# Kernel tuning notes

Hardware: AMD Instinct MI355X
Metric: run time of the kernel (lower is better)

## Reference

```python
import jax, jax.numpy as jnp
import numpy as np

B, L, D = 4, 1024, 1024
H, DK, DV = 16, 64, 64
HID = 4 * D
EPS = 1e-5


def layer_norm(x, w, b):
    m = x.mean(-1, keepdims=True)
    v = ((x - m) ** 2).mean(-1, keepdims=True)
    return (x - m) * jax.lax.rsqrt(v + EPS) * w + b


def sln(hl, w, ln_w, ln_b, gamma, beta):
    # Self-modulated LayerNorm: gamma * w * LN(hl) + beta * w
    return gamma * w * layer_norm(hl, ln_w, ln_b) + beta * w


def setup_inputs() -> dict:
    key = jax.random.key(0)
    ks = jax.random.split(key, 20)
    s = 0.02
    inp = {
        "q": jax.random.normal(ks[0], (B, L, D), jnp.float32),
        "k": jax.random.normal(ks[1], (B, L, D), jnp.float32),
        "v": jax.random.normal(ks[2], (B, L, D), jnp.float32),
        "z": jax.random.normal(ks[3], (B, L, D), jnp.float32),
        # projections stored [in, out] (torch Linear applies x @ W.T + b)
        "wq_w": jax.random.normal(ks[4], (D, H * DK), jnp.float32) * s,
        "wq_b": jnp.zeros((H * DK,), jnp.float32),
        "wk_w": jax.random.normal(ks[5], (D, H * DK), jnp.float32) * s,
        "wk_b": jnp.zeros((H * DK,), jnp.float32),
        "wv_w": jax.random.normal(ks[6], (D, H * DV), jnp.float32) * s,
        "wv_b": jnp.zeros((H * DV,), jnp.float32),
        "fc_w": jax.random.normal(ks[7], (H * DV, D), jnp.float32) * s,
        "fc_b": jnp.zeros((D,), jnp.float32),
        "mlp1_w": jax.random.normal(ks[8], (D, HID), jnp.float32) * s,
        "mlp1_b": jnp.zeros((HID,), jnp.float32),
        "mlp2_w": jax.random.normal(ks[9], (HID, D), jnp.float32) * s,
        "mlp2_b": jnp.zeros((D,), jnp.float32),
        "ln1_w": jnp.ones((D,), jnp.float32),
        "ln1_b": jnp.zeros((D,), jnp.float32),
        "g1": jax.random.normal(ks[10], (1, 1, 1), jnp.float32),
        "b1": jax.random.normal(ks[11], (1, 1, 1), jnp.float32),
        "ln2_w": jnp.ones((D,), jnp.float32),
        "ln2_b": jnp.zeros((D,), jnp.float32),
        "g2": jax.random.normal(ks[12], (1, 1, 1), jnp.float32),
        "b2": jax.random.normal(ks[13], (1, 1, 1), jnp.float32),
    }
    return inp


def reference(q, k, v, z,
              wq_w, wq_b, wk_w, wk_b, wv_w, wv_b, fc_w, fc_b,
              mlp1_w, mlp1_b, mlp2_w, mlp2_b,
              ln1_w, ln1_b, g1, b1, ln2_w, ln2_b, g2, b2):
    scale = 1.0 / np.sqrt(DK).astype(np.float32)
    q = sln(q, z, ln1_w, ln1_b, g1, b1)
    residual = q
    qh = (q @ wq_w + wq_b).reshape(B, L, H, DK)
    kh = (k @ wk_w + wk_b).reshape(B, L, H, DK)
    vh = (v @ wv_w + wv_b).reshape(B, L, H, DV)
    # scores per (head, batch) matching torch layout (n_head*sz_b, Lq, Lk)
    attn = jnp.einsum("bqhd,bkhd->hbqk", qh, kh) * scale
    attn = jax.nn.softmax(attn, axis=-1)
    out = jnp.einsum("hbqk,bkhd->bqhd", attn, vh).reshape(B, L, H * DV)
    out = out @ fc_w + fc_b
    out = out + residual
    h = sln(out, z, ln2_w, ln2_b, g2, b2)
    h = jax.nn.gelu(h @ mlp1_w + mlp1_b, approximate=False)
    out = (h @ mlp2_w + mlp2_b) + out
    return out, attn.reshape(H * B, L, L)
```

## Files before the change

kernel.cpp:

```cpp
#include <hip/hip_runtime.h>
#include <math.h>

namespace {

constexpr int kL  = 1024;
constexpr int kD  = 1024;
constexpr int kB  = 4;
constexpr int kH  = 16;
constexpr int kDK = 64;
constexpr int kHID = 4096;

typedef unsigned short ushort_t;
typedef short  s16x8 __attribute__((ext_vector_type(8)));
typedef float  f32x4 __attribute__((ext_vector_type(4)));
typedef unsigned short u16x4 __attribute__((ext_vector_type(4)));

__device__ __forceinline__ ushort_t f2bf(float f) {
    unsigned u = __float_as_uint(f);
    unsigned r = u + 0x7fffu + ((u >> 16) & 1u);
    return (ushort_t)(r >> 16);
}

__device__ __forceinline__ void gld16(const void* g, void* l) {
    __builtin_amdgcn_global_load_lds((__attribute__((address_space(1))) void*)(g),
                                     (__attribute__((address_space(3))) void*)(l),
                                     16, 0, 0);
}

__device__ __forceinline__ float wred_sum(float v) {
    #pragma unroll
    for (int o = 32; o > 0; o >>= 1) v += __shfl_xor(v, o, 64);
    return v;
}

__global__ __launch_bounds__(256) void prep(
    const float* __restrict__ wq_w, const float* __restrict__ wk_w,
    const float* __restrict__ wv_w, const float* __restrict__ fc_w,
    ushort_t* __restrict__ wT4,
    const float* __restrict__ mlp1_w, ushort_t* __restrict__ m1T,
    const float* __restrict__ mlp2_w, ushort_t* __restrict__ m2T,
    const float* __restrict__ kx, const float* __restrict__ vx, ushort_t* __restrict__ kv,
    const float* __restrict__ q, const float* __restrict__ z,
    const float* __restrict__ ln1w, const float* __restrict__ ln1b,
    const float* __restrict__ g1, const float* __restrict__ b1,
    float* __restrict__ qp, ushort_t* __restrict__ qb)
{
    __shared__ float t[32][33];
    __shared__ float r1[4], r2[4];
    const int b = blockIdx.x;
    const int tid = threadIdx.x;
    if (b < 12288) {
        const float* src; ushort_t* dst; int R, C, bx, by;
        if (b < 4096) {
            int zz = b >> 10, idx = b & 1023;
            src = zz == 0 ? wq_w : zz == 1 ? wk_w : zz == 2 ? wv_w : fc_w;
            dst = wT4 + (size_t)zz * 1048576;
            R = 1024; C = 1024; bx = idx & 31; by = idx >> 5;
        } else if (b < 8192) {
            int idx = b - 4096;
            src = mlp1_w; dst = m1T; R = 1024; C = 4096;
            bx = idx & 127; by = idx >> 7;
        } else {
            int idx = b - 8192;
            src = mlp2_w; dst = m2T; R = 4096; C = 1024;
            bx = idx & 31; by = idx >> 5;
        }
        int c0 = bx * 32, rr0 = by * 32;
        int tx = tid & 31, ty = tid >> 5;
        #pragma unroll
        for (int i = 0; i < 4; i++) {
            int r = ty + i * 8;
            t[r][tx] = src[(size_t)(rr0 + r) * C + c0 + tx];
        }
        __syncthreads();
        #pragma unroll
        for (int i = 0; i < 4; i++) {
            int c = ty + i * 8;
            dst[(size_t)(c0 + c) * R + rr0 + tx] = f2bf(t[tx][c]);
        }
        return;
    }
    if (b < 20480) {
        int bb = b - 12288;
        bool isv = bb >= 4096;
        const float* src = isv ? vx : kx;
        ushort_t* dst = kv + (isv ? (size_t)4194304 : 0);
        int i = (bb & 4095) * 256 + tid;
        f32x4 v = ((const f32x4*)src)[i];
        u16x4 o; o[0] = f2bf(v[0]); o[1] = f2bf(v[1]); o[2] = f2bf(v[2]); o[3] = f2bf(v[3]);
        ((u16x4*)dst)[i] = o;
        return;
    }
    {
        const int row = b - 20480;
        const size_t base = (size_t)row * kD;
        float4 xv = ((const float4*)(q + base))[tid];
        float s  = xv.x + xv.y + xv.z + xv.w;
        float sq = xv.x * xv.x + xv.y * xv.y + xv.z * xv.z + xv.w * xv.w;
        float ws = wred_sum(s), wq = wred_sum(sq);
        int lane = tid & 63, wid = tid >> 6;
        if (lane == 0) { r1[wid] = ws; r2[wid] = wq; }
        __syncthreads();
        float st = r1[0] + r1[1] + r1[2] + r1[3];
        float qt = r2[0] + r2[1] + r2[2] + r2[3];
        float mean = st * (1.0f / kD);
        float var  = qt * (1.0f / kD) - mean * mean;
        float rs = rsqrtf(var + 1e-5f);
        float gv = g1[0], bv = b1[0];
        float4 zv = ((const float4*)(z + base))[tid];
        float4 wv = ((const float4*)ln1w)[tid];
        float4 lb = ((const float4*)ln1b)[tid];
        float4 o;
        o.x = zv.x * (gv * ((xv.x - mean) * rs * wv.x + lb.x) + bv);
        o.y = zv.y * (gv * ((xv.y - mean) * rs * wv.y + lb.y) + bv);
        o.z = zv.z * (gv * ((xv.z - mean) * rs * wv.z + lb.z) + bv);
        o.w = zv.w * (gv * ((xv.w - mean) * rs * wv.w + lb.w) + bv);
        ((float4*)(qp + base))[tid] = o;
        u16x4 ob; ob[0] = f2bf(o.x); ob[1] = f2bf(o.y); ob[2] = f2bf(o.z); ob[3] = f2bf(o.w);
        ((u16x4*)(qb + base))[tid] = ob;
    }
}

__global__ __launch_bounds__(256) void sln_kernel(
    const float* __restrict__ x, const float* __restrict__ x2, float* __restrict__ xw,
    const float* __restrict__ z,
    const float* __restrict__ lnw, const float* __restrict__ lnb,
    const float* __restrict__ g, const float* __restrict__ bt,
    float* __restrict__ outf, ushort_t* __restrict__ outb)
{
    const int row = blockIdx.x;
    const int tid = threadIdx.x;
    const size_t base = (size_t)row * kD;
    float4 xv = ((const float4*)(x + base))[tid];
    if (x2) {
        float4 a = ((const float4*)(x2 + base))[tid];
        xv.x += a.x; xv.y += a.y; xv.z += a.z; xv.w += a.w;
    }
    if (xw) ((float4*)(xw + base))[tid] = xv;
    float s  = xv.x + xv.y + xv.z + xv.w;
    float sq = xv.x * xv.x + xv.y * xv.y + xv.z * xv.z + xv.w * xv.w;
    __shared__ float r1[4], r2[4];
    float ws = wred_sum(s), wq = wred_sum(sq);
    int lane = tid & 63, wid = tid >> 6;
    if (lane == 0) { r1[wid] = ws; r2[wid] = wq; }
    __syncthreads();
    float st = r1[0] + r1[1] + r1[2] + r1[3];
    float qt = r2[0] + r2[1] + r2[2] + r2[3];
    float mean = st * (1.0f / kD);
    float var  = qt * (1.0f / kD) - mean * mean;
    float rs = rsqrtf(var + 1e-5f);
    float gv = g[0], bv = bt[0];
    float4 zv = ((const float4*)(z + base))[tid];
    float4 wv = ((const float4*)lnw)[tid];
    float4 lb = ((const float4*)lnb)[tid];
    float4 o;
    o.x = zv.x * (gv * ((xv.x - mean) * rs * wv.x + lb.x) + bv);
    o.y = zv.y * (gv * ((xv.y - mean) * rs * wv.y + lb.y) + bv);
    o.z = zv.z * (gv * ((xv.z - mean) * rs * wv.z + lb.z) + bv);
    o.w = zv.w * (gv * ((xv.w - mean) * rs * wv.w + lb.w) + bv);
    if (outf) ((float4*)(outf + base))[tid] = o;
    u16x4 ob; ob[0] = f2bf(o.x); ob[1] = f2bf(o.y); ob[2] = f2bf(o.z); ob[3] = f2bf(o.w);
    ((u16x4*)(outb + base))[tid] = ob;
}

__global__ __launch_bounds__(256) void addf4(
    float* __restrict__ dst, const float* __restrict__ src)
{
    int i = blockIdx.x * 256 + threadIdx.x;
    f32x4 d = ((const f32x4*)dst)[i];
    f32x4 s = ((const f32x4*)src)[i];
    d[0] += s[0]; d[1] += s[1]; d[2] += s[2]; d[3] += s[3];
    ((f32x4*)dst)[i] = d;
}

__global__ __launch_bounds__(256) void mgemm(
    const ushort_t* __restrict__ A, int lda,
    const ushort_t* __restrict__ Bt, int ldb,
    void* __restrict__ Cv, int ldc, int K,
    const float* __restrict__ bias, const float* __restrict__ res,
    float scale, int flags, int mode,
    const float* __restrict__ bias1, void* __restrict__ Cv2)
{
    __shared__ __align__(16) ushort_t As[128 * 32];
    __shared__ __align__(16) ushort_t Bs[128 * 32];
    if (mode == 2) {
        int zz = blockIdx.z;
        A  += (size_t)zz * (4096u * 1024u);
        Bt += (size_t)zz * (1024u * 1024u);
        Cv = (void*)((ushort_t*)Cv + (size_t)zz * (4096u * 1024u));
        if (zz == 1) bias = bias1;
    } else if (mode == 3) {
        int zz = blockIdx.z;
        A  += (size_t)zz * K;
        Bt += (size_t)zz * K;
        if (zz == 1) { Cv = Cv2; bias = nullptr; res = nullptr; flags = 0; }
    }
    float*    Cf = (float*)Cv;
    ushort_t* Cb = (ushort_t*)Cv;
    const int nx = gridDim.x, nwg = nx * gridDim.y;
    int f = blockIdx.y * nx + blockIdx.x;
    int rr = (f & 7) * (nwg >> 3) + (f >> 3);
    const int bx = rr % nx, by = rr / nx;
    const int tid = threadIdx.x;
    const int lane = tid & 63, w = tid >> 6;
    const int m0 = by * 128, n0 = bx * 128;
    const int r0 = tid >> 2;
    const int c0 = (tid & 3) ^ (r0 & 3);
    const ushort_t* Ag0 = A  + (size_t)(m0 + r0) * lda + c0 * 8;
    const ushort_t* Ag1 = Ag0 + (size_t)64 * lda;
    const ushort_t* Bg0 = Bt + (size_t)(n0 + r0) * ldb + c0 * 8;
    const ushort_t* Bg1 = Bg0 + (size_t)64 * ldb;
    char* AsW = (char*)As + w * 1024;
    char* BsW = (char*)Bs + w * 1024;
    const int wm = (w & 1) * 64, wn = (w >> 1) * 64;
    const int fn = lane & 15, q = lane >> 4;
    int aoff[4], boff[4];
    #pragma unroll
    for (int i = 0; i < 4; i++) {
        int ra = wm + i * 16 + fn;
        aoff[i] = (ra * 4 + (q ^ (ra & 3))) * 16;
        int rb = wn + i * 16 + fn;
        boff[i] = (rb * 4 + (q ^ (rb & 3))) * 16;
    }
    f32x4 acc[4][4] = {};
    for (int k0 = 0; k0 < K; k0 += 32) {
        gld16(Ag0 + k0, AsW);
        gld16(Ag1 + k0, AsW + 4096);
        gld16(Bg0 + k0, BsW);
        gld16(Bg1 + k0, BsW + 4096);
        __syncthreads();
        s16x8 af[4], bfr[4];
        #pragma unroll
        for (int i = 0; i < 4; i++) {
            af[i]  = *(const s16x8*)((const char*)As + aoff[i]);
            bfr[i] = *(const s16x8*)((const char*)Bs + boff[i]);
        }
        #pragma unroll
        for (int mi = 0; mi < 4; mi++)
            #pragma unroll
            for (int ni = 0; ni < 4; ni++)
                acc[mi][ni] = __builtin_amdgcn_mfma_f32_16x16x32_bf16(
                    af[mi], bfr[ni], acc[mi][ni], 0, 0, 0);
        __syncthreads();
    }
    #pragma unroll
    for (int mi = 0; mi < 4; mi++) {
        #pragma unroll
        for (int ni = 0; ni < 4; ni++) {
            #pragma unroll
            for (int r = 0; r < 4; r++) {
                int gm = m0 + wm + mi * 16 + q * 4 + r;
                int gn = n0 + wn + ni * 16 + fn;
                float v = acc[mi][ni][r] * scale;
                if (bias) v += (flags & 4) ? bias[gm] : bias[gn];
                if (flags & 1) v = 0.5f * v * (1.0f + erff(v * 0.70710678118654752f));
                if (res) v += res[(size_t)gm * ldc + gn];
                if (flags & 2) Cb[(size_t)gm * ldc + gn] = f2bf(v);
                else           Cf[(size_t)gm * ldc + gn] = v;
            }
        }
    }
}

__global__ __launch_bounds__(512) void fused_attn(
    const ushort_t* __restrict__ qh, const ushort_t* __restrict__ kh,
    const ushort_t* __restrict__ vT, float* __restrict__ attn,
    ushort_t* __restrict__ ctx)
{
    __shared__ __align__(16) char PlBuf[8 * 4096];
    __shared__ float redm[8][32];
    __shared__ float reds[8][32];
    const int orig = blockIdx.y * 32 + blockIdx.x;
    const int nf = (orig & 7) * 256 + (orig >> 3);
    const int p = nf >> 5, b = p & 3, h = p >> 2;
    const int m0 = (nf & 31) * 32;
    const int tid = threadIdx.x;
    const int lane = tid & 63, w = tid >> 6;
    const int fn = lane & 15, q = lane >> 4;
    const ushort_t* Qb = qh + (size_t)b * (kL * kD) + h * 64;
    const ushort_t* Kb = kh + (size_t)b * (kL * kD) + h * 64;
    float* Pp = attn + (size_t)p * kL * kL;

    f32x4 acc[2][8] = {};
    #pragma unroll
    for (int kk = 0; kk < 2; kk++) {
        s16x8 aq[2], bq[8];
        #pragma unroll
        for (int mi = 0; mi < 2; mi++)
            aq[mi] = *(const s16x8*)(Qb + (size_t)(m0 + mi * 16 + fn) * kD + kk * 32 + q * 8);
        #pragma unroll
        for (int ni = 0; ni < 8; ni++)
            bq[ni] = *(const s16x8*)(Kb + (size_t)(w * 128 + ni * 16 + fn) * kD + kk * 32 + q * 8);
        #pragma unroll
        for (int mi = 0; mi < 2; mi++)
            #pragma unroll
            for (int ni = 0; ni < 8; ni++)
                acc[mi][ni] = __builtin_amdgcn_mfma_f32_16x16x32_bf16(
                    aq[mi], bq[ni], acc[mi][ni], 0, 0, 0);
    }

    float mloc[2][4];
    #pragma unroll
    for (int mi = 0; mi < 2; mi++) {
        #pragma unroll
        for (int r = 0; r < 4; r++) {
            float m = -3.0e38f;
            #pragma unroll
            for (int ni = 0; ni < 8; ni++) {
                acc[mi][ni][r] *= 0.125f;
                m = fmaxf(m, acc[mi][ni][r]);
            }
            mloc[mi][r] = m;
        }
    }
    #pragma unroll
    for (int o = 1; o < 16; o <<= 1) {
        #pragma unroll
        for (int mi = 0; mi < 2; mi++)
            #pragma unroll
            for (int r = 0; r < 4; r++)
                mloc[mi][r] = fmaxf(mloc[mi][r], __shfl_xor(mloc[mi][r], o, 64));
    }
    if (fn == 0) {
        #pragma unroll
        for (int mi = 0; mi < 2; mi++)
            #pragma unroll
            for (int r = 0; r < 4; r++)
                redm[w][mi * 16 + q * 4 + r] = mloc[mi][r];
    }
    __syncthreads();
    #pragma unroll
    for (int mi = 0; mi < 2; mi++) {
        #pragma unroll
        for (int r = 0; r < 4; r++) {
            int row = mi * 16 + q * 4 + r;
            float m = redm[0][row];
            #pragma unroll
            for (int w2 = 1; w2 < 8; w2++) m = fmaxf(m, redm[w2][row]);
            float s = 0.f;
            #pragma unroll
            for (int ni = 0; ni < 8; ni++) {
                float e = __expf(acc[mi][ni][r] - m);
                acc[mi][ni][r] = e;
                s += e;
            }
            mloc[mi][r] = s;
        }
    }
    #pragma unroll
    for (int o = 1; o < 16; o <<= 1) {
        #pragma unroll
        for (int mi = 0; mi < 2; mi++)
            #pragma unroll
            for (int r = 0; r < 4; r++)
                mloc[mi][r] += __shfl_xor(mloc[mi][r], o, 64);
    }
    if (fn == 0) {
        #pragma unroll
        for (int mi = 0; mi < 2; mi++)
            #pragma unroll
            for (int r = 0; r < 4; r++)
                reds[w][mi * 16 + q * 4 + r] = mloc[mi][r];
    }
    __syncthreads();
    float inv[2][4];
    #pragma unroll
    for (int mi = 0; mi < 2; mi++) {
        #pragma unroll
        for (int r = 0; r < 4; r++) {
            int row = mi * 16 + q * 4 + r;
            float s = reds[0][row];
            #pragma unroll
            for (int w2 = 1; w2 < 8; w2++) s += reds[w2][row];
            inv[mi][r] = 1.0f / s;
        }
    }
    #pragma unroll
    for (int mi = 0; mi < 2; mi++)
        #pragma unroll
        for (int ni = 0; ni < 8; ni++)
            #pragma unroll
            for (int r = 0; r < 4; r++)
                __builtin_nontemporal_store(
                    acc[mi][ni][r] * inv[mi][r],
                    &Pp[(size_t)(m0 + mi * 16 + q * 4 + r) * kL + w * 128 + ni * 16 + fn]);

    const ushort_t* Vb = vT + (size_t)h * 64 * 4096 + (size_t)b * 1024;
    char* Plw = PlBuf + w * 4096;
    f32x4 acc2[2][4] = {};
    #pragma unroll
    for (int half = 0; half < 2; half++) {
        #pragma unroll
        for (int mi = 0; mi < 2; mi++)
            #pragma unroll
            for (int ni = 0; ni < 4; ni++)
                #pragma unroll
                for (int r = 0; r < 4; r++) {
                    int row = mi * 16 + q * 4 + r;
                    int cl  = ni * 16 + fn;
                    *(ushort_t*)(Plw + ((row * 128 + cl * 2) ^ ((row & 7) << 4)))
                        = f2bf(acc[mi][half * 4 + ni][r]);
                }
        #pragma unroll
        for (int kh2 = 0; kh2 < 2; kh2++) {
            int kk = half * 2 + kh2;
            s16x8 pa[2];
            #pragma unroll
            for (int mi = 0; mi < 2; mi++) {
                int row = mi * 16 + fn;
                pa[mi] = *(const s16x8*)(Plw +
                    ((row * 128 + (kh2 * 32 + q * 8) * 2) ^ ((row & 7) << 4)));
            }
            #pragma unroll
            for (int nj = 0; nj < 4; nj++) {
                s16x8 bv = *(const s16x8*)(Vb + (size_t)(nj * 16 + fn) * 4096 +
                                           w * 128 + kk * 32 + q * 8);
                #pragma unroll
                for (int mi = 0; mi < 2; mi++)
                    acc2[mi][nj] = __builtin_amdgcn_mfma_f32_16x16x32_bf16(
                        pa[mi], bv, acc2[mi][nj], 0, 0, 0);
            }
        }
    }
    #pragma unroll
    for (int mi = 0; mi < 2; mi++)
        #pragma unroll
        for (int nj = 0; nj < 4; nj++)
            #pragma unroll
            for (int r = 0; r < 4; r++)
                acc2[mi][nj][r] *= inv[mi][r];

    __syncthreads();
    float (*cred)[2048] = (float (*)[2048])PlBuf;
    if (w < 4) {
        #pragma unroll
        for (int mi = 0; mi < 2; mi++)
            #pragma unroll
            for (int nj = 0; nj < 4; nj++)
                #pragma unroll
                for (int r = 0; r < 4; r++)
                    cred[w][(mi * 16 + q * 4 + r) * 64 + nj * 16 + fn] = acc2[mi][nj][r];
    }
    __syncthreads();
    if (w >= 4) {
        #pragma unroll
        for (int mi = 0; mi < 2; mi++)
            #pragma unroll
            for (int nj = 0; nj < 4; nj++)
                #pragma unroll
                for (int r = 0; r < 4; r++)
                    cred[w - 4][(mi * 16 + q * 4 + r) * 64 + nj * 16 + fn] += acc2[mi][nj][r];
    }
    __syncthreads();
    {
        int idx0 = tid * 4;
        int row = idx0 >> 6, d0 = idx0 & 63;
        f32x4 s0 = *(const f32x4*)&cred[0][idx0];
        #pragma unroll
        for (int wb = 1; wb < 4; wb++) {
            f32x4 t = *(const f32x4*)&cred[wb][idx0];
            s0[0] += t[0]; s0[1] += t[1]; s0[2] += t[2]; s0[3] += t[3];
        }
        u16x4 o;
        o[0] = f2bf(s0[0]); o[1] = f2bf(s0[1]); o[2] = f2bf(s0[2]); o[3] = f2bf(s0[3]);
        *(u16x4*)(ctx + (size_t)b * (kL * kD) + (size_t)(m0 + row) * kD + h * 64 + d0) = o;
    }
}

}

extern "C" void kernel_launch(void* const* d_in, const int* in_sizes, int n_in,
                              void* d_out, int out_size, void* d_ws, size_t ws_size,
                              hipStream_t stream)
{
    (void)in_sizes; (void)n_in; (void)out_size; (void)ws_size;
    const float* q      = (const float*)d_in[0];
    const float* k      = (const float*)d_in[1];
    const float* v      = (const float*)d_in[2];
    const float* z      = (const float*)d_in[3];
    const float* wq_b   = (const float*)d_in[5];
    const float* wq_w   = (const float*)d_in[4];
    const float* wk_w   = (const float*)d_in[6];
    const float* wk_b   = (const float*)d_in[7];
    const float* wv_w   = (const float*)d_in[8];
    const float* wv_b   = (const float*)d_in[9];
    const float* fc_w   = (const float*)d_in[10];
    const float* fc_b   = (const float*)d_in[11];
    const float* mlp1_w = (const float*)d_in[12];
    const float* mlp1_b = (const float*)d_in[13];
    const float* mlp2_w = (const float*)d_in[14];
    const float* mlp2_b = (const float*)d_in[15];
    const float* ln1_w  = (const float*)d_in[16];
    const float* ln1_b  = (const float*)d_in[17];
    const float* g1     = (const float*)d_in[18];
    const float* b1     = (const float*)d_in[19];
    const float* ln2_w  = (const float*)d_in[20];
    const float* ln2_b  = (const float*)d_in[21];
    const float* g2     = (const float*)d_in[22];
    const float* b2     = (const float*)d_in[23];

    float* out0 = (float*)d_out;
    float* attn = (float*)d_out + (size_t)kB * kL * kD;

    char* arena = (char*)d_ws;
    const size_t MB = 1u << 20;
    float*    qp   = (float*)(arena);
    ushort_t* qb   = (ushort_t*)(arena + 16 * MB);
    ushort_t* kb   = (ushort_t*)(arena + 24 * MB);
    ushort_t* vb   = (ushort_t*)(arena + 32 * MB);
    ushort_t* qh   = (ushort_t*)(arena + 40 * MB);
    ushort_t* kh   = (ushort_t*)(arena + 48 * MB);
    ushort_t* vT   = (ushort_t*)(arena + 56 * MB);
    ushort_t* ctx  = (ushort_t*)(arena + 32 * MB);
    float*    fcP  = (float*)(arena + 16 * MB);
    ushort_t* h2   = (ushort_t*)(arena + 32 * MB);
    float*    out1 = (float*)(arena + 64 * MB);
    ushort_t* hid  = (ushort_t*)(arena);
    float*    m2P  = (float*)(arena + 40 * MB);
    ushort_t* wT4  = (ushort_t*)(arena + 80 * MB);
    ushort_t* wvT  = (ushort_t*)(arena + 84 * MB);
    ushort_t* fcT  = (ushort_t*)(arena + 86 * MB);
    ushort_t* m1T  = (ushort_t*)(arena + 88 * MB);
    ushort_t* m2T  = (ushort_t*)(arena + 96 * MB);

    dim3 blk(256);
    prep<<<dim3(24576), blk, 0, stream>>>(wq_w, wk_w, wv_w, fc_w, wT4,
                                          mlp1_w, m1T, mlp2_w, m2T,
                                          k, v, kb,
                                          q, z, ln1_w, ln1_b, g1, b1, qp, qb);
    mgemm<<<dim3(8, 32, 2), blk, 0, stream>>>(qb, kD, wT4, kD, qh, kD, kD,
                                              wq_b, nullptr, 1.0f, 2, 2, wk_b, nullptr);
    mgemm<<<dim3(32, 8, 1), blk, 0, stream>>>(wvT, kD, vb, kD, vT, 4096, kD,
                                              wv_b, nullptr, 1.0f, 2 | 4, 0, nullptr, nullptr);
    fused_attn<<<dim3(kL / 32, 64), dim3(512), 0, stream>>>(qh, kh, vT, attn, ctx);
    mgemm<<<dim3(8, 32, 2), blk, 0, stream>>>(ctx, kD, fcT, kD, out1, kD, kD / 2,
                                              fc_b, qp, 1.0f, 0, 3, nullptr, fcP);
    sln_kernel<<<dim3(kB * kL), blk, 0, stream>>>(out1, fcP, out1, z,
                                                  ln2_w, ln2_b, g2, b2, nullptr, h2);
    mgemm<<<dim3(32, 32, 1), blk, 0, stream>>>(h2, kD, m1T, kD, hid, kHID, kD,
                                               mlp1_b, nullptr, 1.0f, 3, 0, nullptr, nullptr);
    mgemm<<<dim3(8, 32, 2), blk, 0, stream>>>(hid, kHID, m2T, kHID, out0, kD, kHID / 2,
                                              mlp2_b, out1, 1.0f, 0, 3, nullptr, m2P);
    addf4<<<dim3(4096), blk, 0, stream>>>(out0, m2P);
}
```

Before: 798.3 us.

## Widen GEMM K-tile to 64 and batch V projection with Q/K

The mgemm kernel now stages a 64-wide K slice per iteration, with a wider XOR swizzle, in place of 32. This halves the barrier and loop overhead per MFMA and doubles LDS usage. The V projection is folded into the batched Q/K GEMM as a third z-slice with its own bias. A small LDS transpose kernel then produces the per-head transposed V layout the attention kernel reads, replacing the separate transposed-output GEMM. Workspace buffers are re-aliased to fit the new vh/vhT tensors.

```diff
diff --git a/kernel.cpp b/kernel.cpp
--- a/kernel.cpp
+++ b/kernel.cpp
@@ -173,22 +173,46 @@
     ((f32x4*)dst)[i] = d;
 }
 
+__global__ __launch_bounds__(256) void vtrans(
+    const ushort_t* __restrict__ vh, ushort_t* __restrict__ vhT)
+{
+    __shared__ ushort_t t[32][33];
+    int p = blockIdx.z, b = p & 3, h = p >> 2;
+    int j0 = blockIdx.x * 32, d0 = blockIdx.y * 32;
+    int tx = threadIdx.x & 31, ty = threadIdx.x >> 5;
+    const ushort_t* src = vh + (size_t)b * (kL * kD) + h * kDK;
+    #pragma unroll
+    for (int i = 0; i < 4; i++) {
+        int j = ty + i * 8;
+        t[j][tx] = src[(size_t)(j0 + j) * kD + d0 + tx];
+    }
+    __syncthreads();
+    ushort_t* dst = vhT + (size_t)p * (kDK * kL);
+    #pragma unroll
+    for (int i = 0; i < 4; i++) {
+        int d = ty + i * 8;
+        dst[(size_t)(d0 + d) * kL + j0 + tx] = t[tx][d];
+    }
+}
+
 __global__ __launch_bounds__(256) void mgemm(
     const ushort_t* __restrict__ A, int lda,
     const ushort_t* __restrict__ Bt, int ldb,
     void* __restrict__ Cv, int ldc, int K,
     const float* __restrict__ bias, const float* __restrict__ res,
     float scale, int flags, int mode,
-    const float* __restrict__ bias1, void* __restrict__ Cv2)
-{
-    __shared__ __align__(16) ushort_t As[128 * 32];
-    __shared__ __align__(16) ushort_t Bs[128 * 32];
+    const float* __restrict__ bias1, const float* __restrict__ bias2,
+    void* __restrict__ Cv2)
+{
+    __shared__ __align__(16) ushort_t As[128 * 64];
+    __shared__ __align__(16) ushort_t Bs[128 * 64];
     if (mode == 2) {
         int zz = blockIdx.z;
         A  += (size_t)zz * (4096u * 1024u);
         Bt += (size_t)zz * (1024u * 1024u);
         Cv = (void*)((ushort_t*)Cv + (size_t)zz * (4096u * 1024u));
         if (zz == 1) bias = bias1;
+        else if (zz == 2) bias = bias2;
     } else if (mode == 3) {
         int zz = blockIdx.z;
         A  += (size_t)zz * K;
@@ -204,43 +228,48 @@
     const int tid = threadIdx.x;
     const int lane = tid & 63, w = tid >> 6;
     const int m0 = by * 128, n0 = bx * 128;
-    const int r0 = tid >> 2;
-    const int c0 = (tid & 3) ^ (r0 & 3);
+    const int r0 = tid >> 3;
+    const int c0 = (tid & 7) ^ (r0 & 7);
     const ushort_t* Ag0 = A  + (size_t)(m0 + r0) * lda + c0 * 8;
-    const ushort_t* Ag1 = Ag0 + (size_t)64 * lda;
     const ushort_t* Bg0 = Bt + (size_t)(n0 + r0) * ldb + c0 * 8;
-    const ushort_t* Bg1 = Bg0 + (size_t)64 * ldb;
     char* AsW = (char*)As + w * 1024;
     char* BsW = (char*)Bs + w * 1024;
     const int wm = (w & 1) * 64, wn = (w >> 1) * 64;
     const int fn = lane & 15, q = lane >> 4;
-    int aoff[4], boff[4];
+    int abase[4], bbase[4], xoff[2];
     #pragma unroll
     for (int i = 0; i < 4; i++) {
-        int ra = wm + i * 16 + fn;
-        aoff[i] = (ra * 4 + (q ^ (ra & 3))) * 16;
-        int rb = wn + i * 16 + fn;
-        boff[i] = (rb * 4 + (q ^ (rb & 3))) * 16;
-    }
+        abase[i] = (wm + i * 16 + fn) * 128;
+        bbase[i] = (wn + i * 16 + fn) * 128;
+    }
+    #pragma unroll
+    for (int ks = 0; ks < 2; ks++) xoff[ks] = ((ks * 4 + q) ^ (fn & 7)) << 4;
     f32x4 acc[4][4] = {};
-    for (int k0 = 0; k0 < K; k0 += 32) {
+    for (int k0 = 0; k0 < K; k0 += 64) {
         gld16(Ag0 + k0, AsW);
-        gld16(Ag1 + k0, AsW + 4096);
+        gld16(Ag0 + (size_t)32 * lda + k0, AsW + 4096);
+        gld16(Ag0 + (size_t)64 * lda + k0, AsW + 8192);
+        gld16(Ag0 + (size_t)96 * lda + k0, AsW + 12288);
         gld16(Bg0 + k0, BsW);
-        gld16(Bg1 + k0, BsW + 4096);
+        gld16(Bg0 + (size_t)32 * ldb + k0, BsW + 4096);
+        gld16(Bg0 + (size_t)64 * ldb + k0, BsW + 8192);
+        gld16(Bg0 + (size_t)96 * ldb + k0, BsW + 12288);
         __syncthreads();
-        s16x8 af[4], bfr[4];
-        #pragma unroll
-        for (int i = 0; i < 4; i++) {
-            af[i]  = *(const s16x8*)((const char*)As + aoff[i]);
-            bfr[i] = *(const s16x8*)((const char*)Bs + boff[i]);
-        }
-        #pragma unroll
-        for (int mi = 0; mi < 4; mi++)
-            #pragma unroll
-            for (int ni = 0; ni < 4; ni++)
-                acc[mi][ni] = __builtin_amdgcn_mfma_f32_16x16x32_bf16(
-                    af[mi], bfr[ni], acc[mi][ni], 0, 0, 0);
+        #pragma unroll
+        for (int ks = 0; ks < 2; ks++) {
+            s16x8 af[4], bfr[4];
+            #pragma unroll
+            for (int i = 0; i < 4; i++) {
+                af[i]  = *(const s16x8*)((const char*)As + abase[i] + xoff[ks]);
+                bfr[i] = *(const s16x8*)((const char*)Bs + bbase[i] + xoff[ks]);
+            }
+            #pragma unroll
+            for (int mi = 0; mi < 4; mi++)
+                #pragma unroll
+                for (int ni = 0; ni < 4; ni++)
+                    acc[mi][ni] = __builtin_amdgcn_mfma_f32_16x16x32_bf16(
+                        af[mi], bfr[ni], acc[mi][ni], 0, 0, 0);
+        }
         __syncthreads();
     }
     #pragma unroll
@@ -252,7 +281,7 @@
                 int gm = m0 + wm + mi * 16 + q * 4 + r;
                 int gn = n0 + wn + ni * 16 + fn;
                 float v = acc[mi][ni][r] * scale;
-                if (bias) v += (flags & 4) ? bias[gm] : bias[gn];
+                if (bias) v += bias[gn];
                 if (flags & 1) v = 0.5f * v * (1.0f + erff(v * 0.70710678118654752f));
                 if (res) v += res[(size_t)gm * ldc + gn];
                 if (flags & 2) Cb[(size_t)gm * ldc + gn] = f2bf(v);
@@ -264,7 +293,7 @@
 
 __global__ __launch_bounds__(512) void fused_attn(
     const ushort_t* __restrict__ qh, const ushort_t* __restrict__ kh,
-    const ushort_t* __restrict__ vT, float* __restrict__ attn,
+    const ushort_t* __restrict__ vhT, float* __restrict__ attn,
     ushort_t* __restrict__ ctx)
 {
     __shared__ __align__(16) char PlBuf[8 * 4096];
@@ -385,7 +414,7 @@
                     acc[mi][ni][r] * inv[mi][r],
                     &Pp[(size_t)(m0 + mi * 16 + q * 4 + r) * kL + w * 128 + ni * 16 + fn]);
 
-    const ushort_t* Vb = vT + (size_t)h * 64 * 4096 + (size_t)b * 1024;
+    const ushort_t* Vb = vhT + (size_t)p * (kDK * kL);
     char* Plw = PlBuf + w * 4096;
     f32x4 acc2[2][4] = {};
     #pragma unroll
@@ -413,7 +442,7 @@
             }
             #pragma unroll
             for (int nj = 0; nj < 4; nj++) {
-                s16x8 bv = *(const s16x8*)(Vb + (size_t)(nj * 16 + fn) * 4096 +
+                s16x8 bv = *(const s16x8*)(Vb + (size_t)(nj * 16 + fn) * kL +
                                            w * 128 + kk * 32 + q * 8);
                 #pragma unroll
                 for (int mi = 0; mi < 2; mi++)
@@ -478,8 +507,8 @@
     const float* k      = (const float*)d_in[1];
     const float* v      = (const float*)d_in[2];
     const float* z      = (const float*)d_in[3];
+    const float* wq_w   = (const float*)d_in[4];
     const float* wq_b   = (const float*)d_in[5];
-    const float* wq_w   = (const float*)d_in[4];
     const float* wk_w   = (const float*)d_in[6];
     const float* wk_b   = (const float*)d_in[7];
     const float* wv_w   = (const float*)d_in[8];
@@ -510,15 +539,15 @@
     ushort_t* vb   = (ushort_t*)(arena + 32 * MB);
     ushort_t* qh   = (ushort_t*)(arena + 40 * MB);
     ushort_t* kh   = (ushort_t*)(arena + 48 * MB);
-    ushort_t* vT   = (ushort_t*)(arena + 56 * MB);
-    ushort_t* ctx  = (ushort_t*)(arena + 32 * MB);
+    ushort_t* vh   = (ushort_t*)(arena + 56 * MB);
+    ushort_t* vhT  = (ushort_t*)(arena + 32 * MB);
+    ushort_t* ctx  = (ushort_t*)(arena + 56 * MB);
     float*    fcP  = (float*)(arena + 16 * MB);
     ushort_t* h2   = (ushort_t*)(arena + 32 * MB);
     float*    out1 = (float*)(arena + 64 * MB);
     ushort_t* hid  = (ushort_t*)(arena);
     float*    m2P  = (float*)(arena + 40 * MB);
     ushort_t* wT4  = (ushort_t*)(arena + 80 * MB);
-    ushort_t* wvT  = (ushort_t*)(arena + 84 * MB);
     ushort_t* fcT  = (ushort_t*)(arena + 86 * MB);
     ushort_t* m1T  = (ushort_t*)(arena + 88 * MB);
     ushort_t* m2T  = (ushort_t*)(arena + 96 * MB);
@@ -528,18 +557,17 @@
                                           mlp1_w, m1T, mlp2_w, m2T,
                                           k, v, kb,
                                           q, z, ln1_w, ln1_b, g1, b1, qp, qb);
-    mgemm<<<dim3(8, 32, 2), blk, 0, stream>>>(qb, kD, wT4, kD, qh, kD, kD,
-                                              wq_b, nullptr, 1.0f, 2, 2, wk_b, nullptr);
-    mgemm<<<dim3(32, 8, 1), blk, 0, stream>>>(wvT, kD, vb, kD, vT, 4096, kD,
-                                              wv_b, nullptr, 1.0f, 2 | 4, 0, nullptr, nullptr);
-    fused_attn<<<dim3(kL / 32, 64), dim3(512), 0, stream>>>(qh, kh, vT, attn, ctx);
+    mgemm<<<dim3(8, 32, 3), blk, 0, stream>>>(qb, kD, wT4, kD, qh, kD, kD,
+                                              wq_b, nullptr, 1.0f, 2, 2, wk_b, wv_b, nullptr);
+    vtrans<<<dim3(32, 2, 64), blk, 0, stream>>>(vh, vhT);
+    fused_attn<<<dim3(kL / 32, 64), dim3(512), 0, stream>>>(qh, kh, vhT, attn, ctx);
     mgemm<<<dim3(8, 32, 2), blk, 0, stream>>>(ctx, kD, fcT, kD, out1, kD, kD / 2,
-                                              fc_b, qp, 1.0f, 0, 3, nullptr, fcP);
+                                              fc_b, qp, 1.0f, 0, 3, nullptr, nullptr, fcP);
     sln_kernel<<<dim3(kB * kL), blk, 0, stream>>>(out1, fcP, out1, z,
                                                   ln2_w, ln2_b, g2, b2, nullptr, h2);
     mgemm<<<dim3(32, 32, 1), blk, 0, stream>>>(h2, kD, m1T, kD, hid, kHID, kD,
-                                               mlp1_b, nullptr, 1.0f, 3, 0, nullptr, nullptr);
+                                               mlp1_b, nullptr, 1.0f, 3, 0, nullptr, nullptr, nullptr);
     mgemm<<<dim3(8, 32, 2), blk, 0, stream>>>(hid, kHID, m2T, kHID, out0, kD, kHID / 2,
-                                              mlp2_b, out1, 1.0f, 0, 3, nullptr, m2P);
+                                              mlp2_b, out1, 1.0f, 0, 3, nullptr, nullptr, m2P);
     addf4<<<dim3(4096), blk, 0, stream>>>(out0, m2P);
 }
```

Result: faster. 753.9 us (-5.6%).
